# Optimization experiments

Hardware: AMD Instinct MI355X
Metric: run time of the kernel (lower is better)

## Reference

```python
import jax, jax.numpy as jnp
import numpy as np

M1, N1, M2, N2 = 32, 64, 24, 48  # Kronecker block dims; 32*24=768, 64*48=3072


def setup_inputs() -> dict:
    key = jax.random.key(0)
    k1, k2, k3, k4, k5 = jax.random.split(key, 5)
    rank = 64
    x = jax.random.normal(k1, (4, 4096, 768), dtype=jnp.float32)
    A_factors = jax.random.normal(k2, (M1 * N1, rank), dtype=jnp.float32) * 0.05
    B_factors = jax.random.normal(k3, (rank, M2 * N2), dtype=jnp.float32) * 0.05
    # 'Sparse' residual is materialized dense in the original module (to_dense()).
    Sparse = jax.random.normal(k4, (768, 3072), dtype=jnp.float32) * 0.02
    bias = jax.random.normal(k5, (3072,), dtype=jnp.float32) * 0.02
    return {"x": x, "A_factors": A_factors, "B_factors": B_factors,
            "Sparse": Sparse, "bias": bias}


def reference(x, A_factors, B_factors, Sparse, bias):
    # Low-rank product: [2048, r] @ [r, 1152] -> [2048, 1152]
    W_tilde = A_factors @ B_factors
    # Kronecker permute: (m1, n1, m2, n2) -> (m1, m2, n1, n2) -> [768, 3072]
    W_low = W_tilde.reshape(M1, N1, M2, N2).transpose(0, 2, 1, 3).reshape(
        M1 * M2, N1 * N2)
    W = W_low + Sparse
    # Dense GEMM: [B, S, 768] @ [768, 3072] + bias
    return x @ W + bias
```

## Files before the change

kernel.cpp:

```cpp
#include <hip/hip_runtime.h>
#include <hip/hip_bf16.h>
#include <stdint.h>

#define M_TOT 16384
#define N_TOT 3072
#define K_TOT 768

#define BM 256
#define BN 256
#define BK 32
#define NT (K_TOT / BK)

typedef __attribute__((ext_vector_type(8))) short short8;
typedef __attribute__((ext_vector_type(4))) float f32x4;

__device__ __forceinline__ unsigned short f2bf(float f) {
    union { float f; unsigned u; } v;
    v.f = f;
    unsigned r = v.u + 0x7FFFu + ((v.u >> 16) & 1u);
    return (unsigned short)(r >> 16);
}

__global__ __launch_bounds__(384) void prep_cvt_kernel(
    const float* __restrict__ Af, const float* __restrict__ Bf,
    const float* __restrict__ Sp, const float* __restrict__ x,
    unsigned short* __restrict__ xb, unsigned short* __restrict__ Wt) {
    __shared__ float a_sh[4][64];
    __shared__ float wrow[4][1160];
    const int tid = threadIdx.x;
    const int b = blockIdx.x;

    if (b < 512) {
        const int m1 = b >> 4;
        const int n10 = (b & 15) * 4;
        if (tid < 256) {
            int rr = tid >> 6, k = tid & 63;
            a_sh[rr][k] = Af[(size_t)(m1 * 64 + n10 + rr) * 64 + k];
        }
        __syncthreads();
        float acc[4][3] = {};
        #pragma unroll 2
        for (int k = 0; k < 64; ++k) {
            const float* brow = Bf + (size_t)k * 1152;
            float b0 = brow[tid], b1 = brow[tid + 384], b2 = brow[tid + 768];
            #pragma unroll
            for (int rr = 0; rr < 4; ++rr) {
                float a = a_sh[rr][k];
                acc[rr][0] = fmaf(a, b0, acc[rr][0]);
                acc[rr][1] = fmaf(a, b1, acc[rr][1]);
                acc[rr][2] = fmaf(a, b2, acc[rr][2]);
            }
        }
        #pragma unroll
        for (int rr = 0; rr < 4; ++rr) {
            wrow[rr][tid] = acc[rr][0];
            wrow[rr][tid + 384] = acc[rr][1];
            wrow[rr][tid + 768] = acc[rr][2];
        }
        __syncthreads();
        if (tid < 192) {
            const int rr = tid / 48, n2 = tid % 48;
            const int c = (n10 + rr) * 48 + n2;
            const int r0 = m1 * 24;
            unsigned w[12];
            #pragma unroll
            for (int t2 = 0; t2 < 12; ++t2) {
                float lo = wrow[rr][(2 * t2) * 48 + n2]
                         + Sp[(size_t)(r0 + 2 * t2) * 3072 + c];
                float hi = wrow[rr][(2 * t2 + 1) * 48 + n2]
                         + Sp[(size_t)(r0 + 2 * t2 + 1) * 3072 + c];
                w[t2] = (unsigned)f2bf(lo) | ((unsigned)f2bf(hi) << 16);
            }
            uint4* d4 = reinterpret_cast<uint4*>(Wt + (size_t)c * 768 + r0);
            d4[0] = (uint4){w[0], w[1], w[2], w[3]};
            d4[1] = (uint4){w[4], w[5], w[6], w[7]};
            d4[2] = (uint4){w[8], w[9], w[10], w[11]};
        }
    } else {
        const int n8 = M_TOT * K_TOT / 8;
        int i = (b - 512) * 384 + tid;
        const int stride = 2048 * 384;
        const float4* xv = reinterpret_cast<const float4*>(x);
        uint4* ov = reinterpret_cast<uint4*>(xb);
        for (; i < n8; i += stride) {
            float4 a = xv[2 * i], c = xv[2 * i + 1];
            uint4 o;
            o.x = (unsigned)f2bf(a.x) | ((unsigned)f2bf(a.y) << 16);
            o.y = (unsigned)f2bf(a.z) | ((unsigned)f2bf(a.w) << 16);
            o.z = (unsigned)f2bf(c.x) | ((unsigned)f2bf(c.y) << 16);
            o.w = (unsigned)f2bf(c.z) | ((unsigned)f2bf(c.w) << 16);
            ov[i] = o;
        }
    }
}

__device__ __forceinline__ void gld16(const void* g, void* l) {
    __builtin_amdgcn_global_load_lds(
        (const __attribute__((address_space(1))) void*)g,
        (__attribute__((address_space(3))) void*)l, 16, 0, 0);
}

__global__ __launch_bounds__(512, 2) void gemm_bt_kernel(
    const unsigned short* __restrict__ A, const unsigned short* __restrict__ Bt,
    const float* __restrict__ bias, float* __restrict__ C) {
    __shared__ unsigned short As[4][BM * BK];
    __shared__ unsigned short Bs[4][BN * BK];

    const int tid = threadIdx.x;
    const int lane = tid & 63;
    const int wid = tid >> 6;
    const int wr = wid >> 2;
    const int wc = wid & 3;

    const int wg = (blockIdx.x & 7) * 96 + (blockIdx.x >> 3);
    const int bm = wg / (N_TOT / BN), bn = wg % (N_TOT / BN);
    const int brow = bm * BM, bcol = bn * BN;

    const int srow = tid >> 2;
    const int soff = (((tid & 3) ^ ((tid >> 3) & 3)) << 4);
    const char* pA = (const char*)A + ((size_t)(brow + srow) * K_TOT) * 2 + soff;
    const char* pB = (const char*)Bt + ((size_t)(bcol + srow) * K_TOT) * 2 + soff;
    const size_t row128 = (size_t)128 * K_TOT * 2;
    const int tid16 = tid * 16;

#define STAGE_AH(u) do { const char* s_ = pA + (size_t)(u) * (BK * 2);           \
        gld16(s_,          (char*)&As[(u) & 3][0] + tid16);                      \
        gld16(s_ + row128, (char*)&As[(u) & 3][0] + tid16 + 8192); } while (0)
#define STAGE_BH(u) do { const char* s_ = pB + (size_t)(u) * (BK * 2);           \
        gld16(s_,          (char*)&Bs[(u) & 3][0] + tid16);                      \
        gld16(s_ + row128, (char*)&Bs[(u) & 3][0] + tid16 + 8192); } while (0)

    const int la = lane & 15;
    const int g4 = lane >> 4;
    const int swb = ((g4 ^ ((lane >> 1) & 3)) << 4);
#define FRAG_A(bu, r) (*(const short8*)((const char*)&As[bu][0] + (r) * 64 + swb))
#define FRAG_B(bu, r) (*(const short8*)((const char*)&Bs[bu][0] + (r) * 64 + swb))

    f32x4 acc[8][4];
    #pragma unroll
    for (int m = 0; m < 8; ++m)
        #pragma unroll
        for (int n = 0; n < 4; ++n)
            acc[m][n] = (f32x4){0.f, 0.f, 0.f, 0.f};

    const int arow = wr * 128;
    const int bcolw = wc * 64;

    short8 bE[4], bO[4], aLo[4], aHi[4];

    STAGE_AH(0); STAGE_BH(0);
    STAGE_AH(1); STAGE_BH(1);
    STAGE_AH(2); STAGE_BH(2);
    asm volatile("s_waitcnt vmcnt(4)" ::: "memory");
    __builtin_amdgcn_s_barrier();
    #pragma unroll
    for (int n = 0; n < 4; ++n) bE[n] = FRAG_B(0, bcolw + n * 16 + la);
    #pragma unroll
    for (int m = 0; m < 4; ++m) aLo[m] = FRAG_A(0, arow + m * 16 + la);
    __builtin_amdgcn_sched_barrier(0);

    auto tile_body = [&](int t, short8 (&bc)[4], short8 (&bnx)[4]) {
        const int bu = t & 3;
        #pragma unroll
        for (int m = 0; m < 4; ++m) aHi[m] = FRAG_A(bu, arow + 64 + m * 16 + la);
        if (t < NT - 3) STAGE_AH(t + 3);
        __builtin_amdgcn_sched_barrier(0);
        __builtin_amdgcn_s_barrier();
        __builtin_amdgcn_s_setprio(1);
        #pragma unroll
        for (int m = 0; m < 4; ++m)
            #pragma unroll
            for (int n = 0; n < 4; ++n)
                acc[m][n] = __builtin_amdgcn_mfma_f32_16x16x32_bf16(
                    bc[n], aLo[m], acc[m][n], 0, 0, 0);
        __builtin_amdgcn_s_setprio(0);
        if (t < NT - 1) {
            const int bu1 = (t + 1) & 3;
            #pragma unroll
            for (int n = 0; n < 4; ++n) bnx[n] = FRAG_B(bu1, bcolw + n * 16 + la);
            #pragma unroll
            for (int m = 0; m < 4; ++m) aLo[m] = FRAG_A(bu1, arow + m * 16 + la);
        }
        if (t < NT - 3) STAGE_BH(t + 3);
        __builtin_amdgcn_sched_barrier(0);
        if (t < NT - 3)       asm volatile("s_waitcnt vmcnt(4)" ::: "memory");
        else if (t == NT - 3) asm volatile("s_waitcnt vmcnt(0)" ::: "memory");
        __builtin_amdgcn_s_barrier();
        __builtin_amdgcn_s_setprio(1);
        #pragma unroll
        for (int m = 0; m < 4; ++m)
            #pragma unroll
            for (int n = 0; n < 4; ++n)
                acc[4 + m][n] = __builtin_amdgcn_mfma_f32_16x16x32_bf16(
                    bc[n], aHi[m], acc[4 + m][n], 0, 0, 0);
        __builtin_amdgcn_s_setprio(0);
    };

    #pragma unroll 1
    for (int tt = 0; tt < NT; tt += 2) {
        tile_body(tt, bE, bO);
        tile_body(tt + 1, bO, bE);
    }

    #pragma unroll
    for (int n = 0; n < 4; ++n) {
        const int gc = bcol + bcolw + n * 16 + g4 * 4;
        const f32x4 bv = *reinterpret_cast<const f32x4*>(&bias[gc]);
        #pragma unroll
        for (int m = 0; m < 8; ++m) {
            const int gr = brow + arow + m * 16 + la;
            f32x4 o = {acc[m][n][0] + bv[0], acc[m][n][1] + bv[1],
                       acc[m][n][2] + bv[2], acc[m][n][3] + bv[3]};
            *reinterpret_cast<f32x4*>(&C[(size_t)gr * N_TOT + gc]) = o;
        }
    }
#undef STAGE_AH
#undef STAGE_BH
#undef FRAG_A
#undef FRAG_B
}

extern "C" void kernel_launch(void* const* d_in, const int* in_sizes, int n_in,
                              void* d_out, int out_size, void* d_ws, size_t ws_size,
                              hipStream_t stream) {
    const float* x    = (const float*)d_in[0];
    const float* Af   = (const float*)d_in[1];
    const float* Bf   = (const float*)d_in[2];
    const float* Sp   = (const float*)d_in[3];
    const float* bias = (const float*)d_in[4];
    float* out = (float*)d_out;

    unsigned short* xb = (unsigned short*)d_ws;
    unsigned short* wt = xb + (size_t)M_TOT * K_TOT;

    hipLaunchKernelGGL(prep_cvt_kernel, dim3(512 + 2048), dim3(384), 0, stream,
                       Af, Bf, Sp, x, xb, wt);
    hipLaunchKernelGGL(gemm_bt_kernel,
                       dim3((M_TOT / BM) * (N_TOT / BN)), dim3(512),
                       0, stream, xb, wt, bias, out);
}
```

Baseline: 122.5 us.

## Make GEMM persistent over three column tiles with prefetch overlapping the epilogue

```diff
diff --git a/kernel.cpp b/kernel.cpp
--- a/kernel.cpp
+++ b/kernel.cpp
@@ -112,16 +112,18 @@
     const int wr = wid >> 2;
     const int wc = wid & 3;
 
-    const int wg = (blockIdx.x & 7) * 96 + (blockIdx.x >> 3);
-    const int bm = wg / (N_TOT / BN), bn = wg % (N_TOT / BN);
-    const int brow = bm * BM, bcol = bn * BN;
+    const int b = blockIdx.x;
+    const int xcd = b & 7, loc = b >> 3;
+    const int bm = xcd * 8 + (loc >> 2);
+    const int q = loc & 3;
+    const int brow = bm * BM;
 
     const int srow = tid >> 2;
     const int soff = (((tid & 3) ^ ((tid >> 3) & 3)) << 4);
     const char* pA = (const char*)A + ((size_t)(brow + srow) * K_TOT) * 2 + soff;
-    const char* pB = (const char*)Bt + ((size_t)(bcol + srow) * K_TOT) * 2 + soff;
     const size_t row128 = (size_t)128 * K_TOT * 2;
     const int tid16 = tid * 16;
+    const char* pB;
 
 #define STAGE_AH(u) do { const char* s_ = pA + (size_t)(u) * (BK * 2);           \
         gld16(s_,          (char*)&As[(u) & 3][0] + tid16);                      \
@@ -137,81 +139,105 @@
 #define FRAG_B(bu, r) (*(const short8*)((const char*)&Bs[bu][0] + (r) * 64 + swb))
 
     f32x4 acc[8][4];
-    #pragma unroll
-    for (int m = 0; m < 8; ++m)
-        #pragma unroll
-        for (int n = 0; n < 4; ++n)
-            acc[m][n] = (f32x4){0.f, 0.f, 0.f, 0.f};
-
     const int arow = wr * 128;
     const int bcolw = wc * 64;
-
     short8 bE[4], bO[4], aLo[4], aHi[4];
 
+    int bcol = q * 3 * BN;
+    pB = (const char*)Bt + ((size_t)(bcol + srow) * K_TOT) * 2 + soff;
     STAGE_AH(0); STAGE_BH(0);
     STAGE_AH(1); STAGE_BH(1);
     STAGE_AH(2); STAGE_BH(2);
     asm volatile("s_waitcnt vmcnt(4)" ::: "memory");
     __builtin_amdgcn_s_barrier();
-    #pragma unroll
-    for (int n = 0; n < 4; ++n) bE[n] = FRAG_B(0, bcolw + n * 16 + la);
-    #pragma unroll
-    for (int m = 0; m < 4; ++m) aLo[m] = FRAG_A(0, arow + m * 16 + la);
-    __builtin_amdgcn_sched_barrier(0);
-
-    auto tile_body = [&](int t, short8 (&bc)[4], short8 (&bnx)[4]) {
-        const int bu = t & 3;
-        #pragma unroll
-        for (int m = 0; m < 4; ++m) aHi[m] = FRAG_A(bu, arow + 64 + m * 16 + la);
-        if (t < NT - 3) STAGE_AH(t + 3);
+
+    #pragma unroll 1
+    for (int it = 0; it < 3; ++it) {
+        const bool bnd = (it != 0);
+
+        #pragma unroll
+        for (int m = 0; m < 8; ++m)
+            #pragma unroll
+            for (int n = 0; n < 4; ++n)
+                acc[m][n] = (f32x4){0.f, 0.f, 0.f, 0.f};
+
+        #pragma unroll
+        for (int n = 0; n < 4; ++n) bE[n] = FRAG_B(0, bcolw + n * 16 + la);
+        #pragma unroll
+        for (int m = 0; m < 4; ++m) aLo[m] = FRAG_A(0, arow + m * 16 + la);
         __builtin_amdgcn_sched_barrier(0);
-        __builtin_amdgcn_s_barrier();
-        __builtin_amdgcn_s_setprio(1);
-        #pragma unroll
-        for (int m = 0; m < 4; ++m)
-            #pragma unroll
-            for (int n = 0; n < 4; ++n)
-                acc[m][n] = __builtin_amdgcn_mfma_f32_16x16x32_bf16(
-                    bc[n], aLo[m], acc[m][n], 0, 0, 0);
-        __builtin_amdgcn_s_setprio(0);
-        if (t < NT - 1) {
-            const int bu1 = (t + 1) & 3;
-            #pragma unroll
-            for (int n = 0; n < 4; ++n) bnx[n] = FRAG_B(bu1, bcolw + n * 16 + la);
-            #pragma unroll
-            for (int m = 0; m < 4; ++m) aLo[m] = FRAG_A(bu1, arow + m * 16 + la);
-        }
-        if (t < NT - 3) STAGE_BH(t + 3);
-        __builtin_amdgcn_sched_barrier(0);
-        if (t < NT - 3)       asm volatile("s_waitcnt vmcnt(4)" ::: "memory");
-        else if (t == NT - 3) asm volatile("s_waitcnt vmcnt(0)" ::: "memory");
-        __builtin_amdgcn_s_barrier();
-        __builtin_amdgcn_s_setprio(1);
-        #pragma unroll
-        for (int m = 0; m < 4; ++m)
-            #pragma unroll
-            for (int n = 0; n < 4; ++n)
-                acc[4 + m][n] = __builtin_amdgcn_mfma_f32_16x16x32_bf16(
-                    bc[n], aHi[m], acc[4 + m][n], 0, 0, 0);
-        __builtin_amdgcn_s_setprio(0);
-    };
-
-    #pragma unroll 1
-    for (int tt = 0; tt < NT; tt += 2) {
-        tile_body(tt, bE, bO);
-        tile_body(tt + 1, bO, bE);
-    }
-
-    #pragma unroll
-    for (int n = 0; n < 4; ++n) {
-        const int gc = bcol + bcolw + n * 16 + g4 * 4;
-        const f32x4 bv = *reinterpret_cast<const f32x4*>(&bias[gc]);
-        #pragma unroll
-        for (int m = 0; m < 8; ++m) {
-            const int gr = brow + arow + m * 16 + la;
-            f32x4 o = {acc[m][n][0] + bv[0], acc[m][n][1] + bv[1],
-                       acc[m][n][2] + bv[2], acc[m][n][3] + bv[3]};
-            *reinterpret_cast<f32x4*>(&C[(size_t)gr * N_TOT + gc]) = o;
+
+        auto tile_body = [&](int t, short8 (&bc)[4], short8 (&bnx)[4]) {
+            const int bu = t & 3;
+            #pragma unroll
+            for (int m = 0; m < 4; ++m)
+                aHi[m] = FRAG_A(bu, arow + 64 + m * 16 + la);
+            if (t < NT - 3) STAGE_AH(t + 3);
+            __builtin_amdgcn_sched_barrier(0);
+            __builtin_amdgcn_s_setprio(1);
+            #pragma unroll
+            for (int m = 0; m < 4; ++m)
+                #pragma unroll
+                for (int n = 0; n < 4; ++n)
+                    acc[m][n] = __builtin_amdgcn_mfma_f32_16x16x32_bf16(
+                        bc[n], aLo[m], acc[m][n], 0, 0, 0);
+            __builtin_amdgcn_s_setprio(0);
+            if (t < NT - 1) {
+                const int bu1 = (t + 1) & 3;
+                #pragma unroll
+                for (int n = 0; n < 4; ++n)
+                    bnx[n] = FRAG_B(bu1, bcolw + n * 16 + la);
+                #pragma unroll
+                for (int m = 0; m < 4; ++m)
+                    aLo[m] = FRAG_A(bu1, arow + m * 16 + la);
+            }
+            if (t < NT - 3) STAGE_BH(t + 3);
+            __builtin_amdgcn_sched_barrier(0);
+            if (t == 0 && bnd)    asm volatile("s_waitcnt vmcnt(36)" ::: "memory");
+            else if (t < NT - 3)  asm volatile("s_waitcnt vmcnt(4)" ::: "memory");
+            else if (t == NT - 3) asm volatile("s_waitcnt vmcnt(0)" ::: "memory");
+            __builtin_amdgcn_s_barrier();
+            __builtin_amdgcn_s_setprio(1);
+            #pragma unroll
+            for (int m = 0; m < 4; ++m)
+                #pragma unroll
+                for (int n = 0; n < 4; ++n)
+                    acc[4 + m][n] = __builtin_amdgcn_mfma_f32_16x16x32_bf16(
+                        bc[n], aHi[m], acc[4 + m][n], 0, 0, 0);
+            __builtin_amdgcn_s_setprio(0);
+        };
+
+        #pragma unroll 1
+        for (int tt = 0; tt < NT; tt += 2) {
+            tile_body(tt, bE, bO);
+            tile_body(tt + 1, bO, bE);
+        }
+
+        const int bcolCur = bcol;
+        if (it < 2) {
+            __builtin_amdgcn_s_barrier();
+            bcol = (q * 3 + it + 1) * BN;
+            pB = (const char*)Bt + ((size_t)(bcol + srow) * K_TOT) * 2 + soff;
+            STAGE_AH(0); STAGE_BH(0);
+            STAGE_AH(1); STAGE_BH(1);
+            STAGE_AH(2); STAGE_BH(2);
+            __builtin_amdgcn_sched_barrier(0);
+        }
+        #pragma unroll
+        for (int n = 0; n < 4; ++n) {
+            const int gc = bcolCur + bcolw + n * 16 + g4 * 4;
+            const f32x4 bv = *reinterpret_cast<const f32x4*>(&bias[gc]);
+            #pragma unroll
+            for (int m = 0; m < 8; ++m) {
+                const int gr = brow + arow + m * 16 + la;
+                f32x4 o = {acc[m][n][0] + bv[0], acc[m][n][1] + bv[1],
+                           acc[m][n][2] + bv[2], acc[m][n][3] + bv[3]};
+                *reinterpret_cast<f32x4*>(&C[(size_t)gr * N_TOT + gc]) = o;
+            }
+        }
+        if (it < 2) {
+            asm volatile("s_waitcnt vmcnt(36)" ::: "memory");
+            __builtin_amdgcn_s_barrier();
         }
     }
 #undef STAGE_AH
@@ -235,7 +261,6 @@
 
     hipLaunchKernelGGL(prep_cvt_kernel, dim3(512 + 2048), dim3(384), 0, stream,
                        Af, Bf, Sp, x, xb, wt);
-    hipLaunchKernelGGL(gemm_bt_kernel,
-                       dim3((M_TOT / BM) * (N_TOT / BN)), dim3(512),
+    hipLaunchKernelGGL(gemm_bt_kernel, dim3(256), dim3(512),
                        0, stream, xb, wt, bias, out);
 }
```

New measurement: 124.5 us. No clear change (+1.6%).
